# Kernel tuning notes

Measured on AMD Instinct MI355X. Metric: run time of the kernel, lower is better.

The kernel has to match this reference:

```python
import jax, jax.numpy as jnp
import numpy as np

B = 2048          # batch_size
C = 128           # num_cells (coarse grid / shift range)
L = 16384         # shape[-1] (mask length)
P = C // 2        # reflect pad on each side


def _interp_linear(x, out_len):
    """F.interpolate(mode='linear', align_corners=False) on last axis.
    x: (..., n) -> (..., out_len)."""
    n = x.shape[-1]
    scale = n / out_len
    pos = jnp.clip((jnp.arange(out_len, dtype=jnp.float32) + 0.5) * scale - 0.5, 0.0, None)
    i0 = jnp.clip(jnp.floor(pos).astype(jnp.int32), 0, n - 1)
    i1 = jnp.minimum(i0 + 1, n - 1)
    w = pos - i0.astype(jnp.float32)
    return x[..., i0] * (1.0 - w) + x[..., i1] * w


def setup_inputs() -> dict:
    key = jax.random.key(0)
    k1, k2, k3 = jax.random.split(key, 3)
    return {
        "logits": 0.1 * jax.random.normal(k1, (C,), dtype=jnp.float32),
        "u": jax.random.uniform(k2, (B, C), dtype=jnp.float32),
        "shift_x": jax.random.randint(k3, (B,), 0, C, dtype=jnp.int32),
    }


def reference(logits, u, shift_x):
    p = jax.nn.sigmoid(logits)                              # (C,)
    grid = (u < p[None, :]).astype(jnp.float32)             # Bernoulli sample, (B, C)
    # Bernoulli log_prob summed over cells, numerically stable via log-sigmoid
    log_probs = (grid * jax.nn.log_sigmoid(logits)
                 + (1.0 - grid) * jax.nn.log_sigmoid(-logits)).sum(axis=1)  # (B,)
    grid_up = _interp_linear(grid[:, None, :], L)           # (B, 1, L)
    padded = jnp.pad(grid_up, ((0, 0), (0, 0), (P, P)), mode="reflect")  # (B, 1, L+2P)
    # vectorized per-sample dynamic shift: masks[b] = padded[b, :, s_b : s_b + L]
    idx = shift_x[:, None, None] + jnp.arange(L, dtype=jnp.int32)[None, None, :]
    masks = jnp.take_along_axis(padded, idx, axis=2)        # (B, 1, L)
    return masks, log_probs
```

## Files before the change

### kernel.cpp

```cpp
#include <hip/hip_runtime.h>
#include <math.h>

constexpr int B   = 2048;
constexpr int C   = 128;
constexpr int L   = 16384;
constexpr int PAD = 64;

__global__ __launch_bounds__(256) void mask_policy_kernel(
    const float* __restrict__ logits,
    const float* __restrict__ u,
    const int*   __restrict__ shift_x,
    float*       __restrict__ out)
{
    __shared__ float  g_sh[C];
    __shared__ float2 bd_sh[C];
    __shared__ float  red_sh[2];

    const int b   = blockIdx.x;
    const int tid = threadIdx.x;

    float lp = 0.0f;
    if (tid < C) {
        float  x  = logits[tid];
        double ed = exp(-(double)x);
        float  p  = (float)(1.0 / (1.0 + ed));
        float  uv = u[(size_t)b * C + tid];
        float  g  = (uv < p) ? 1.0f : 0.0f;
        g_sh[tid] = g;
        float lsp = -log1pf((float)ed);
        float lsn = lsp - x;
        lp = (g != 0.0f) ? lsp : lsn;
    }
    float v = lp;
    #pragma unroll
    for (int off = 32; off > 0; off >>= 1) v += __shfl_down(v, off, 64);
    if (tid == 0)  red_sh[0] = v;
    if (tid == 64) red_sh[1] = v;
    __syncthreads();

    if (tid < C) {
        float g0 = g_sh[tid];
        float g1 = g_sh[(tid < C - 1) ? tid + 1 : C - 1];
        bd_sh[tid] = make_float2(g0, g1 - g0);
    }
    if (tid == 0) out[(size_t)B * L + b] = red_sh[0] + red_sh[1];
    __syncthreads();

    const int shift = shift_x[b];
    const int s  = shift - PAD;
    const int s2 = shift - 2 * PAD;

    auto general = [&](int j) -> float {
        int t = s + j;
        if (t < 0)       t = -t;
        else if (t >= L) t = 2 * L - 2 - t;
        float pos = (t + 0.5f) * (1.0f / 128.0f) - 0.5f;
        pos = fmaxf(pos, 0.0f);
        int i0 = (int)pos;
        if (i0 > C - 1) i0 = C - 1;
        float w = pos - (float)i0;
        float2 bd = bd_sh[i0];
        return fmaf(w, bd.y, bd.x);
    };

    float* orow = out + (size_t)b * L;

    #pragma unroll
    for (int k = 0; k < L / (256 * 4); ++k) {
        const int j0 = (k * 256 + tid) * 4;
        float4 r;
        if (k > 0 && k < 15) {
            const int tm = j0 + s2;
            const int m  = tm >> 7;
            const int rr = tm & 127;
            if (rr <= 124) {
                const float2 bd = bd_sh[m];
                const float w0 = (rr + 0.5f) * (1.0f / 128.0f);
                const float v0 = fmaf(w0, bd.y, bd.x);
                const float st = bd.y * (1.0f / 128.0f);
                r.x = v0;
                r.y = v0 + st;
                r.z = v0 + 2.0f * st;
                r.w = v0 + 3.0f * st;
            } else {
                float vals[4];
                #pragma unroll
                for (int q = 0; q < 4; ++q) {
                    const int tmq = tm + q;
                    const int mq  = tmq >> 7;
                    const int rq  = tmq & 127;
                    const float wq = (rq + 0.5f) * (1.0f / 128.0f);
                    const float2 bd = bd_sh[mq];
                    vals[q] = fmaf(wq, bd.y, bd.x);
                }
                r.x = vals[0]; r.y = vals[1]; r.z = vals[2]; r.w = vals[3];
            }
        } else {
            r.x = general(j0);
            r.y = general(j0 + 1);
            r.z = general(j0 + 2);
            r.w = general(j0 + 3);
        }
        *reinterpret_cast<float4*>(orow + j0) = r;
    }
}

extern "C" void kernel_launch(void* const* d_in, const int* in_sizes, int n_in,
                              void* d_out, int out_size, void* d_ws, size_t ws_size,
                              hipStream_t stream) {
    const float* logits  = (const float*)d_in[0];
    const float* u       = (const float*)d_in[1];
    const int*   shift_x = (const int*)d_in[2];
    float*       out     = (float*)d_out;

    mask_policy_kernel<<<B, 256, 0, stream>>>(logits, u, shift_x, out);
}
```

Before: 26.24 us.

## Process four rows per 1024-thread block and defer log-prob reduction

Each block now handles four batch rows with 256 threads per row, cutting the grid from 2048 to 512 blocks. The precomputed (g0, delta) float2 table and one barrier are removed; neighbours are read straight from a padded per-row grid array. The log-prob warp reduction moves after the mask stores so it no longer delays the write stream. This cuts per-block setup and barriers, but 1024-thread blocks can reduce scheduling flexibility and add an extra LDS read per element.

```diff
diff --git a/kernel.cpp b/kernel.cpp
--- a/kernel.cpp
+++ b/kernel.cpp
@@ -1,83 +1,75 @@
 #include <hip/hip_runtime.h>
 #include <math.h>
 
-constexpr int B   = 2048;
-constexpr int C   = 128;
-constexpr int L   = 16384;
-constexpr int PAD = 64;
+constexpr int B    = 2048;
+constexpr int C    = 128;
+constexpr int L    = 16384;
+constexpr int PAD  = 64;
+constexpr int ROWS = 4;
+constexpr int NBLK = B / ROWS;
 
-__global__ __launch_bounds__(256) void mask_policy_kernel(
+__global__ __launch_bounds__(1024) void mask_policy_kernel(
     const float* __restrict__ logits,
     const float* __restrict__ u,
     const int*   __restrict__ shift_x,
     float*       __restrict__ out)
 {
-    __shared__ float  g_sh[C];
-    __shared__ float2 bd_sh[C];
-    __shared__ float  red_sh[2];
+    __shared__ float g_sh[ROWS][C + 4];
+    __shared__ float red_sh[ROWS][2];
 
-    const int b   = blockIdx.x;
     const int tid = threadIdx.x;
+    const int tg  = tid >> 8;
+    const int t   = tid & 255;
+    const int row = blockIdx.x * ROWS + tg;
+
+    const int shift = shift_x[row];
 
     float lp = 0.0f;
-    if (tid < C) {
-        float  x  = logits[tid];
+    if (t < C) {
+        float  uv = u[(size_t)row * C + t];
+        float  x  = logits[t];
         double ed = exp(-(double)x);
         float  p  = (float)(1.0 / (1.0 + ed));
-        float  uv = u[(size_t)b * C + tid];
         float  g  = (uv < p) ? 1.0f : 0.0f;
-        g_sh[tid] = g;
+        g_sh[tg][t] = g;
+        if (t == C - 1) g_sh[tg][C] = g;
         float lsp = -log1pf((float)ed);
-        float lsn = lsp - x;
-        lp = (g != 0.0f) ? lsp : lsn;
+        lp = (g != 0.0f) ? lsp : (lsp - x);
     }
-    float v = lp;
-    #pragma unroll
-    for (int off = 32; off > 0; off >>= 1) v += __shfl_down(v, off, 64);
-    if (tid == 0)  red_sh[0] = v;
-    if (tid == 64) red_sh[1] = v;
     __syncthreads();
 
-    if (tid < C) {
-        float g0 = g_sh[tid];
-        float g1 = g_sh[(tid < C - 1) ? tid + 1 : C - 1];
-        bd_sh[tid] = make_float2(g0, g1 - g0);
-    }
-    if (tid == 0) out[(size_t)B * L + b] = red_sh[0] + red_sh[1];
-    __syncthreads();
-
-    const int shift = shift_x[b];
     const int s  = shift - PAD;
     const int s2 = shift - 2 * PAD;
+    const float* __restrict__ g = g_sh[tg];
+    float* orow = out + (size_t)row * L;
 
     auto general = [&](int j) -> float {
-        int t = s + j;
-        if (t < 0)       t = -t;
-        else if (t >= L) t = 2 * L - 2 - t;
-        float pos = (t + 0.5f) * (1.0f / 128.0f) - 0.5f;
+        int tt = s + j;
+        if (tt < 0)       tt = -tt;
+        else if (tt >= L) tt = 2 * L - 2 - tt;
+        float pos = (tt + 0.5f) * (1.0f / 128.0f) - 0.5f;
         pos = fmaxf(pos, 0.0f);
         int i0 = (int)pos;
         if (i0 > C - 1) i0 = C - 1;
-        float w = pos - (float)i0;
-        float2 bd = bd_sh[i0];
-        return fmaf(w, bd.y, bd.x);
+        float w  = pos - (float)i0;
+        float g0 = g[i0];
+        float g1 = g[i0 + 1];
+        return fmaf(w, g1 - g0, g0);
     };
 
-    float* orow = out + (size_t)b * L;
-
     #pragma unroll
-    for (int k = 0; k < L / (256 * 4); ++k) {
-        const int j0 = (k * 256 + tid) * 4;
+    for (int k = 0; k < 16; ++k) {
+        const int j0 = (k * 256 + t) * 4;
         float4 r;
         if (k > 0 && k < 15) {
-            const int tm = j0 + s2;
-            const int m  = tm >> 7;
-            const int rr = tm & 127;
+            const int m  = (j0 + s2) >> 7;
+            const int rr = (j0 + s2) & 127;
             if (rr <= 124) {
-                const float2 bd = bd_sh[m];
+                const float g0 = g[m];
+                const float d  = g[m + 1] - g0;
                 const float w0 = (rr + 0.5f) * (1.0f / 128.0f);
-                const float v0 = fmaf(w0, bd.y, bd.x);
-                const float st = bd.y * (1.0f / 128.0f);
+                const float v0 = fmaf(w0, d, g0);
+                const float st = d * (1.0f / 128.0f);
                 r.x = v0;
                 r.y = v0 + st;
                 r.z = v0 + 2.0f * st;
@@ -86,12 +78,12 @@
                 float vals[4];
                 #pragma unroll
                 for (int q = 0; q < 4; ++q) {
-                    const int tmq = tm + q;
+                    const int tmq = j0 + s2 + q;
                     const int mq  = tmq >> 7;
                     const int rq  = tmq & 127;
                     const float wq = (rq + 0.5f) * (1.0f / 128.0f);
-                    const float2 bd = bd_sh[mq];
-                    vals[q] = fmaf(wq, bd.y, bd.x);
+                    const float g0 = g[mq];
+                    vals[q] = fmaf(wq, g[mq + 1] - g0, g0);
                 }
                 r.x = vals[0]; r.y = vals[1]; r.z = vals[2]; r.w = vals[3];
             }
@@ -103,6 +95,14 @@
         }
         *reinterpret_cast<float4*>(orow + j0) = r;
     }
+
+    float v = lp;
+    #pragma unroll
+    for (int off = 32; off > 0; off >>= 1) v += __shfl_down(v, off, 64);
+    if (t == 0)  red_sh[tg][0] = v;
+    if (t == 64) red_sh[tg][1] = v;
+    __syncthreads();
+    if (t == 0) out[(size_t)B * L + row] = red_sh[tg][0] + red_sh[tg][1];
 }
 
 extern "C" void kernel_launch(void* const* d_in, const int* in_sizes, int n_in,
@@ -113,5 +113,5 @@
     const int*   shift_x = (const int*)d_in[2];
     float*       out     = (float*)d_out;
 
-    mask_policy_kernel<<<B, 256, 0, stream>>>(logits, u, shift_x, out);
+    mask_policy_kernel<<<NBLK, 1024, 0, stream>>>(logits, u, shift_x, out);
 }
```

New measurement: 26.13 us. Within noise of the previous version (-0.4%).
